# Kernel tuning notes

Hardware: AMD Instinct MI355X
Metric: run time of the kernel (lower is better)

Reference implementation:

```python
import jax, jax.numpy as jnp
import numpy as np

B, L, D = 2, 1024, 512
E = 2
DI = E * D            # d_inner = 1024
N = 16                # d_state
K = 4                 # d_conv
DT_RANK = 32          # ceil(d_model / 16)


def setup_inputs() -> dict:
    key = jax.random.key(0)
    ks = jax.random.split(key, 12)
    s = lambda i, shape, scale=0.02: jax.random.normal(ks[i], shape, jnp.float32) * scale
    return {
        "x": jax.random.normal(ks[0], (B, L, D), jnp.float32),
        # Mamba params (mamba_ssm layout: Linear weights are [out, in])
        "W_in": s(1, (2 * DI, D)),                 # in_proj, bias=False
        "conv_w": s(2, (DI, K), 0.1),              # depthwise conv kernel
        "conv_b": jnp.zeros((DI,), jnp.float32),
        "W_xproj": s(3, (DT_RANK + 2 * N, DI)),    # x_proj, bias=False
        "W_dt": s(4, (DI, DT_RANK), 0.1),
        "b_dt": s(5, (DI,), 0.5),
        "A_log": jnp.log(jnp.broadcast_to(jnp.arange(1, N + 1, dtype=jnp.float32), (DI, N))),
        "D_skip": jnp.ones((DI,), jnp.float32),
        "W_out": s(6, (D, DI)),                    # out_proj, bias=False
        # block params
        "g1": jnp.ones((D,), jnp.float32), "b1": jnp.zeros((D,), jnp.float32),
        "W_ff1": s(7, (2 * D, D)), "b_ff1": jnp.zeros((2 * D,), jnp.float32),
        "W_ff2": s(8, (D, 2 * D)), "b_ff2": jnp.zeros((D,), jnp.float32),
        "g2": jnp.ones((D,), jnp.float32), "b2": jnp.zeros((D,), jnp.float32),
    }


def layernorm(x, g, b, eps=1e-5):
    m = x.mean(-1, keepdims=True)
    v = jnp.mean(jnp.square(x - m), -1, keepdims=True)
    return (x - m) * jax.lax.rsqrt(v + eps) * g + b


def mamba(x, W_in, conv_w, conv_b, W_xproj, W_dt, b_dt, A_log, D_skip, W_out):
    xz = x @ W_in.T                              # [B,L,2*DI]
    u, z = jnp.split(xz, 2, axis=-1)             # each [B,L,DI]
    # causal depthwise conv1d over time
    u_t = u.transpose(0, 2, 1)                   # [B,DI,L]
    conv = jax.lax.conv_general_dilated(
        u_t, conv_w[:, None, :], (1,), [(K - 1, 0)], feature_group_count=DI)
    u = jax.nn.silu(conv.transpose(0, 2, 1) + conv_b)   # [B,L,DI]
    # input-dependent dt, B, C
    x_dbl = u @ W_xproj.T                        # [B,L,DT_RANK+2N]
    dt_r, Bm, Cm = jnp.split(x_dbl, [DT_RANK, DT_RANK + N], axis=-1)
    dt = jax.nn.softplus(dt_r @ W_dt.T + b_dt)   # [B,L,DI]
    A = -jnp.exp(A_log)                          # [DI,N]
    dA = jnp.exp(dt[..., None] * A)                                # [B,L,DI,N]
    dBu = dt[..., None] * Bm[:, :, None, :] * u[..., None]         # [B,L,DI,N]

    def step(h, xs):
        dA_t, dBu_t, C_t = xs
        h = dA_t * h + dBu_t                    # [B,DI,N]
        y = jnp.einsum('bdn,bn->bd', h, C_t)
        return h, y

    h0 = jnp.zeros((B, DI, N), dt.dtype)
    _, ys = jax.lax.scan(step, h0, (dA.transpose(1, 0, 2, 3),
                                    dBu.transpose(1, 0, 2, 3),
                                    Cm.transpose(1, 0, 2)))
    y = ys.transpose(1, 0, 2) + u * D_skip       # [B,L,DI]
    y = y * jax.nn.silu(z)
    return y @ W_out.T                            # [B,L,D]


def reference(x, W_in, conv_w, conv_b, W_xproj, W_dt, b_dt, A_log, D_skip, W_out,
              g1, b1, W_ff1, b_ff1, W_ff2, b_ff2, g2, b2):
    m = mamba(x, W_in, conv_w, conv_b, W_xproj, W_dt, b_dt, A_log, D_skip, W_out)
    res1 = x - m
    r = layernorm(res1, g1, b1)
    ff = jax.nn.gelu(r @ W_ff1.T + b_ff1, approximate=False) @ W_ff2.T + b_ff2
    res2 = r - ff
    out = layernorm(jax.nn.silu(res2), g2, b2)
    return out + x
```

## Files before the change

kernel.cpp:

```cpp
#include <hip/hip_runtime.h>
#include <math.h>

#define BB 2
#define LL 1024
#define DD 512
#define DIN 1024
#define NS 16
#define RNK 32
#define ML (BB*LL)
#define CT 16
#define NC (LL/CT)
#define BDIN (BB*DIN)

typedef unsigned short u16;
typedef unsigned int u32;

__device__ __forceinline__ float sigmoidf_(float v) { return 1.f / (1.f + __expf(-v)); }
__device__ __forceinline__ float siluf_(float v) { return v * sigmoidf_(v); }
__device__ __forceinline__ u16 f2bf(float f) {
  union { float f; u32 u; } c; c.f = f;
  u32 r = c.u + 0x7fffu + ((c.u >> 16) & 1u);
  return (u16)(r >> 16);
}
__device__ __forceinline__ float bf2f(u16 x) {
  union { u32 u; float f; } c; c.u = (u32)x << 16;
  return c.f;
}

__global__ __launch_bounds__(256) void cast_all(const float* __restrict__ x,
                                                const float* __restrict__ Wi,
                                                const float* __restrict__ Wx,
                                                const float* __restrict__ Wd,
                                                const float* __restrict__ Wo,
                                                const float* __restrict__ Wf1,
                                                const float* __restrict__ Wf2,
                                                u16* bx, u16* bWi, u16* bWx, u16* bWd,
                                                u16* bWo, u16* bWf1, u16* bWf2)
{
  int bid = blockIdx.x;
  const float* src; u16* dst; int base;
  if (bid < 512)       { src = x;   dst = bx;   base = 0; }
  else if (bid < 1024) { src = Wi;  dst = bWi;  base = 512; }
  else if (bid < 1056) { src = Wx;  dst = bWx;  base = 1024; }
  else if (bid < 1072) { src = Wd;  dst = bWd;  base = 1056; }
  else if (bid < 1328) { src = Wo;  dst = bWo;  base = 1072; }
  else if (bid < 1584) { src = Wf1; dst = bWf1; base = 1328; }
  else                 { src = Wf2; dst = bWf2; base = 1584; }
  int i = ((bid - base) * 256 + threadIdx.x) * 8;
  float4 v0 = *(const float4*)&src[i];
  float4 v1 = *(const float4*)&src[i + 4];
  union { u16 u[8]; uint4 v; } p;
  p.u[0] = f2bf(v0.x); p.u[1] = f2bf(v0.y); p.u[2] = f2bf(v0.z); p.u[3] = f2bf(v0.w);
  p.u[4] = f2bf(v1.x); p.u[5] = f2bf(v1.y); p.u[6] = f2bf(v1.z); p.u[7] = f2bf(v1.w);
  *(uint4*)&dst[i] = p.v;
}

using bf16x8 = __attribute__((ext_vector_type(8))) short;
using f32x4  = __attribute__((ext_vector_type(4))) float;

template<int BM, int BN, int EPI, typename OT>
__global__ __launch_bounds__(256) void gemm_t(const u16* __restrict__ A,
                                              const u16* __restrict__ W,
                                              const float* __restrict__ bias,
                                              OT* __restrict__ C,
                                              int M, int N, int K)
{
  constexpr int WR = BM / 64;
  constexpr int WC = 4 / WR;
  constexpr int NW = BN / WC;
  constexpr int JJ = NW / 16;
  constexpr int RB = BN / 64;
  __shared__ u16 As[BM][40];
  __shared__ u16 Bs[BN][40];
  const int bm = blockIdx.y * BM, bn = blockIdx.x * BN;
  const int tid = threadIdx.x;
  const int w = tid >> 6, l = tid & 63;
  const int wr = w / WC, wc = w % WC;
  const int lr = l & 15, lh = l >> 4;
  const int sr0 = tid >> 2, sc0 = tid & 3;
  f32x4 acc[4][JJ] = {};
  for (int k0 = 0; k0 < K; k0 += 32) {
    uint4 areg[WR], breg[RB];
#pragma unroll
    for (int i = 0; i < WR; ++i)
      areg[i] = *(const uint4*)&A[(size_t)(bm + sr0 + 64 * i) * K + k0 + sc0 * 8];
#pragma unroll
    for (int i = 0; i < RB; ++i)
      breg[i] = *(const uint4*)&W[(size_t)(bn + sr0 + 64 * i) * K + k0 + sc0 * 8];
    __syncthreads();
#pragma unroll
    for (int i = 0; i < WR; ++i) *(uint4*)&As[sr0 + 64 * i][sc0 * 8] = areg[i];
#pragma unroll
    for (int i = 0; i < RB; ++i) *(uint4*)&Bs[sr0 + 64 * i][sc0 * 8] = breg[i];
    __syncthreads();
    bf16x8 af[4], bfr[JJ];
#pragma unroll
    for (int i = 0; i < 4; ++i) af[i]  = *(bf16x8*)&As[wr * 64 + i * 16 + lr][lh * 8];
#pragma unroll
    for (int j = 0; j < JJ; ++j) bfr[j] = *(bf16x8*)&Bs[wc * NW + j * 16 + lr][lh * 8];
#pragma unroll
    for (int i = 0; i < 4; ++i)
#pragma unroll
      for (int j = 0; j < JJ; ++j)
        acc[i][j] = __builtin_amdgcn_mfma_f32_16x16x32_bf16(af[i], bfr[j], acc[i][j], 0, 0, 0);
  }
#pragma unroll
  for (int i = 0; i < 4; ++i) {
#pragma unroll
    for (int j = 0; j < JJ; ++j) {
      int col = bn + wc * NW + j * 16 + lr;
      float bv = (EPI >= 1) ? bias[col] : 0.f;
#pragma unroll
      for (int r = 0; r < 4; ++r) {
        int row = bm + wr * 64 + i * 16 + lh * 4 + r;
        float t = acc[i][j][r] + bv;
        if (EPI == 2) t = 0.5f * t * (1.f + erff(t * 0.70710678118654752f));
        if (EPI == 3) t = fmaxf(t, 0.f) + log1pf(__expf(-fabsf(t)));
        if constexpr (sizeof(OT) == 2) C[(size_t)row * N + col] = (OT)f2bf(t);
        else                           C[(size_t)row * N + col] = (OT)t;
      }
    }
  }
}

__global__ __launch_bounds__(256) void xproj_mfma(const u16* __restrict__ A,
                                                  const u16* __restrict__ W,
                                                  float* __restrict__ C,
                                                  u16* __restrict__ bdtr)
{
  __shared__ u16 As[128][40];
  __shared__ u16 Bs[64][40];
  const int bm = blockIdx.x * 128;
  const int tid = threadIdx.x;
  const int w = tid >> 6, l = tid & 63;
  const int lr = l & 15, lh = l >> 4;
  const int sr0 = tid >> 2, sc0 = tid & 3;
  f32x4 acc[2][4] = {};
  for (int k0 = 0; k0 < DIN; k0 += 32) {
    uint4 a0 = *(const uint4*)&A[(size_t)(bm + sr0) * DIN + k0 + sc0 * 8];
    uint4 a1 = *(const uint4*)&A[(size_t)(bm + sr0 + 64) * DIN + k0 + sc0 * 8];
    uint4 b0;
    if (sr0 < 64) b0 = *(const uint4*)&W[(size_t)sr0 * DIN + k0 + sc0 * 8];
    __syncthreads();
    *(uint4*)&As[sr0][sc0 * 8] = a0;
    *(uint4*)&As[sr0 + 64][sc0 * 8] = a1;
    if (sr0 < 64) *(uint4*)&Bs[sr0][sc0 * 8] = b0;
    __syncthreads();
    bf16x8 af[2], bfr[4];
#pragma unroll
    for (int i = 0; i < 2; ++i) af[i]  = *(bf16x8*)&As[w * 32 + i * 16 + lr][lh * 8];
#pragma unroll
    for (int j = 0; j < 4; ++j) bfr[j] = *(bf16x8*)&Bs[j * 16 + lr][lh * 8];
#pragma unroll
    for (int i = 0; i < 2; ++i)
#pragma unroll
      for (int j = 0; j < 4; ++j)
        acc[i][j] = __builtin_amdgcn_mfma_f32_16x16x32_bf16(af[i], bfr[j], acc[i][j], 0, 0, 0);
  }
#pragma unroll
  for (int i = 0; i < 2; ++i)
#pragma unroll
    for (int j = 0; j < 4; ++j) {
      int col = j * 16 + lr;
#pragma unroll
      for (int r = 0; r < 4; ++r) {
        int row = bm + w * 32 + i * 16 + lh * 4 + r;
        float v = acc[i][j][r];
        C[(size_t)row * 64 + col] = v;
        if (j < 2) bdtr[(size_t)row * RNK + col] = f2bf(v);
      }
    }
}

__global__ __launch_bounds__(256) void conv_silu(const float* __restrict__ xz,
                                                 const float* __restrict__ conv_w,
                                                 const float* __restrict__ conv_b,
                                                 u16* __restrict__ ucb)
{
  int idx = blockIdx.x * 256 + threadIdx.x;
  int d = idx & (DIN - 1);
  int bl = idx >> 10;
  int l = bl & (LL - 1);
  int b = bl >> 10;
  float acc = conv_b[d];
#pragma unroll
  for (int k = 0; k < 4; ++k) {
    int ls = l - 3 + k;
    float uv = (ls >= 0) ? xz[((size_t)(b * LL + ls)) * (2 * DIN) + d] : 0.f;
    acc = fmaf(uv, conv_w[d * 4 + k], acc);
  }
  ucb[idx] = f2bf(siluf_(acc));
}


__global__ __launch_bounds__(256) void scan_p1(const float* __restrict__ dt,
                                               const u16* __restrict__ ucb,
                                               const float* __restrict__ xdbl,
                                               const float* __restrict__ A_log,
                                               float* __restrict__ apG,
                                               float* __restrict__ hG)
{
  __shared__ float dts[CT][256];
  __shared__ float us[CT][256];
  __shared__ float Bs[CT][NS];
  const int d0 = blockIdx.x * 256, c = blockIdx.y, b = blockIdx.z;
  const int tid = threadIdx.x;
  const int t0 = c * CT;
  for (int i = tid; i < CT * 64; i += 256) {
    int r = i >> 6, col = (i & 63) * 4;
    size_t row = (size_t)(b * LL + t0 + r);
    *(float4*)&dts[r][col] = *(const float4*)&dt[row * DIN + d0 + col];
    ushort4 uv = *(const ushort4*)&ucb[row * DIN + d0 + col];
    float4 uf = { bf2f(uv.x), bf2f(uv.y), bf2f(uv.z), bf2f(uv.w) };
    *(float4*)&us[r][col] = uf;
  }
  { int r = tid >> 4, n = tid & 15;
    Bs[r][n] = xdbl[(size_t)(b * LL + t0 + r) * 64 + 32 + n]; }
  __syncthreads();
  const int d = d0 + tid;
  float Ad[NS];
#pragma unroll
  for (int n = 0; n < NS; ++n) Ad[n] = -__expf(A_log[d * NS + n]);
  float h[NS] = {};
  float sdt = 0.f;
#pragma unroll 4
  for (int t = 0; t < CT; ++t) {
    float dtv = dts[t][tid];
    float dtu = dtv * us[t][tid];
    sdt += dtv;
    float4 B0 = *(float4*)&Bs[t][0],  B1 = *(float4*)&Bs[t][4];
    float4 B2 = *(float4*)&Bs[t][8],  B3 = *(float4*)&Bs[t][12];
    float Bq[NS] = { B0.x, B0.y, B0.z, B0.w, B1.x, B1.y, B1.z, B1.w,
                     B2.x, B2.y, B2.z, B2.w, B3.x, B3.y, B3.z, B3.w };
#pragma unroll
    for (int n = 0; n < NS; ++n) {
      float a = __expf(dtv * Ad[n]);
      h[n] = fmaf(a, h[n], dtu * Bq[n]);
    }
  }
  const int bd = b * DIN + d;
#pragma unroll
  for (int n = 0; n < NS; ++n) {
    apG[((size_t)c * NS + n) * BDIN + bd] = __expf(Ad[n] * sdt);
    hG [((size_t)c * NS + n) * BDIN + bd] = h[n];
  }
}

__global__ __launch_bounds__(128) void scan_p2(const float* __restrict__ apG,
                                               float* __restrict__ hG)
{
  const int idx = blockIdx.x * 128 + threadIdx.x;
  float H = 0.f;
#pragma unroll 16
  for (int c = 0; c < NC; ++c) {
    size_t o = (size_t)c * (NS * BDIN) + idx;
    float ap = apG[o];
    float hl = hG[o];
    hG[o] = H;
    H = fmaf(ap, H, hl);
  }
}

__global__ __launch_bounds__(256) void scan_p3(const float* __restrict__ dt,
                                               const u16* __restrict__ ucb,
                                               const float* __restrict__ xz,
                                               const float* __restrict__ xdbl,
                                               const float* __restrict__ A_log,
                                               const float* __restrict__ D_skip,
                                               const float* __restrict__ hG,
                                               u16* __restrict__ ygb)
{
  __shared__ float dts[CT][256];
  __shared__ float us[CT][256];
  __shared__ float zs[CT][256];
  __shared__ float Bs[CT][NS];
  __shared__ float Cs[CT][NS];
  const int d0 = blockIdx.x * 256, c = blockIdx.y, b = blockIdx.z;
  const int tid = threadIdx.x;
  const int t0 = c * CT;
  for (int i = tid; i < CT * 64; i += 256) {
    int r = i >> 6, col = (i & 63) * 4;
    size_t row = (size_t)(b * LL + t0 + r);
    *(float4*)&dts[r][col] = *(const float4*)&dt[row * DIN + d0 + col];
    ushort4 uv = *(const ushort4*)&ucb[row * DIN + d0 + col];
    float4 uf = { bf2f(uv.x), bf2f(uv.y), bf2f(uv.z), bf2f(uv.w) };
    *(float4*)&us[r][col] = uf;
    *(float4*)&zs[r][col] = *(const float4*)&xz[row * (2 * DIN) + DIN + d0 + col];
  }
  { int r = tid >> 4, n = tid & 15;
    size_t row = (size_t)(b * LL + t0 + r);
    Bs[r][n] = xdbl[row * 64 + 32 + n];
    Cs[r][n] = xdbl[row * 64 + 48 + n]; }
  __syncthreads();
  const int d = d0 + tid;
  const int bd = b * DIN + d;
  float Ad[NS];
#pragma unroll
  for (int n = 0; n < NS; ++n) Ad[n] = -__expf(A_log[d * NS + n]);
  const float Dd = D_skip[d];
  float h[NS];
#pragma unroll
  for (int n = 0; n < NS; ++n) h[n] = hG[((size_t)c * NS + n) * BDIN + bd];
#pragma unroll 2
  for (int t = 0; t < CT; ++t) {
    float dtv = dts[t][tid];
    float ucv = us[t][tid];
    float dtu = dtv * ucv;
    float4 B0 = *(float4*)&Bs[t][0],  B1 = *(float4*)&Bs[t][4];
    float4 B2 = *(float4*)&Bs[t][8],  B3 = *(float4*)&Bs[t][12];
    float4 C0 = *(float4*)&Cs[t][0],  C1 = *(float4*)&Cs[t][4];
    float4 C2 = *(float4*)&Cs[t][8],  C3 = *(float4*)&Cs[t][12];
    float Bq[NS] = { B0.x, B0.y, B0.z, B0.w, B1.x, B1.y, B1.z, B1.w,
                     B2.x, B2.y, B2.z, B2.w, B3.x, B3.y, B3.z, B3.w };
    float Cq[NS] = { C0.x, C0.y, C0.z, C0.w, C1.x, C1.y, C1.z, C1.w,
                     C2.x, C2.y, C2.z, C2.w, C3.x, C3.y, C3.z, C3.w };
    float y = 0.f;
#pragma unroll
    for (int n = 0; n < NS; ++n) {
      float a = __expf(dtv * Ad[n]);
      h[n] = fmaf(a, h[n], dtu * Bq[n]);
      y = fmaf(h[n], Cq[n], y);
    }
    float o = fmaf(ucv, Dd, y) * siluf_(zs[t][tid]);
    ygb[(size_t)(b * LL + t0 + t) * DIN + d0 + tid] = f2bf(o);
  }
}

__global__ __launch_bounds__(256) void ln1_kernel(const float* __restrict__ x,
                                                  const float* __restrict__ m,
                                                  const float* __restrict__ g,
                                                  const float* __restrict__ b,
                                                  float* __restrict__ r,
                                                  u16* __restrict__ rbf)
{
  int row = blockIdx.x;
  int tid = threadIdx.x;
  size_t base = (size_t)row * DD;
  float2 xv = *(const float2*)&x[base + tid * 2];
  float2 mv = *(const float2*)&m[base + tid * 2];
  float v0 = xv.x - mv.x, v1 = xv.y - mv.y;
  float s = v0 + v1, ss = v0 * v0 + v1 * v1;
#pragma unroll
  for (int off = 32; off; off >>= 1) { s += __shfl_down(s, off, 64); ss += __shfl_down(ss, off, 64); }
  __shared__ float sm[8];
  int w = tid >> 6;
  if ((tid & 63) == 0) { sm[w] = s; sm[4 + w] = ss; }
  __syncthreads();
  float S = sm[0] + sm[1] + sm[2] + sm[3];
  float SS = sm[4] + sm[5] + sm[6] + sm[7];
  float mean = S * (1.f / DD);
  float var = SS * (1.f / DD) - mean * mean;
  float rstd = rsqrtf(var + 1e-5f);
  float2 gv = *(const float2*)&g[tid * 2];
  float2 bv = *(const float2*)&b[tid * 2];
  float2 o;
  o.x = (v0 - mean) * rstd * gv.x + bv.x;
  o.y = (v1 - mean) * rstd * gv.y + bv.y;
  *(float2*)&r[base + tid * 2] = o;
  u32 pk = (u32)f2bf(o.x) | ((u32)f2bf(o.y) << 16);
  *(u32*)&rbf[base + tid * 2] = pk;
}

__global__ __launch_bounds__(256) void final_kernel(const float* __restrict__ r,
                                                    const float* __restrict__ ff,
                                                    const float* __restrict__ x,
                                                    const float* __restrict__ g,
                                                    const float* __restrict__ b,
                                                    float* __restrict__ out)
{
  int row = blockIdx.x;
  int tid = threadIdx.x;
  size_t base = (size_t)row * DD;
  float2 rv = *(const float2*)&r[base + tid * 2];
  float2 fv = *(const float2*)&ff[base + tid * 2];
  float v0 = rv.x - fv.x, v1 = rv.y - fv.y;
  v0 = siluf_(v0); v1 = siluf_(v1);
  float s = v0 + v1, ss = v0 * v0 + v1 * v1;
#pragma unroll
  for (int off = 32; off; off >>= 1) { s += __shfl_down(s, off, 64); ss += __shfl_down(ss, off, 64); }
  __shared__ float sm[8];
  int w = tid >> 6;
  if ((tid & 63) == 0) { sm[w] = s; sm[4 + w] = ss; }
  __syncthreads();
  float S = sm[0] + sm[1] + sm[2] + sm[3];
  float SS = sm[4] + sm[5] + sm[6] + sm[7];
  float mean = S * (1.f / DD);
  float var = SS * (1.f / DD) - mean * mean;
  float rstd = rsqrtf(var + 1e-5f);
  float2 gv = *(const float2*)&g[tid * 2];
  float2 bv = *(const float2*)&b[tid * 2];
  float2 xv = *(const float2*)&x[base + tid * 2];
  float2 o;
  o.x = (v0 - mean) * rstd * gv.x + bv.x + xv.x;
  o.y = (v1 - mean) * rstd * gv.y + bv.y + xv.y;
  *(float2*)&out[base + tid * 2] = o;
}

extern "C" void kernel_launch(void* const* d_in, const int* in_sizes, int n_in,
                              void* d_out, int out_size, void* d_ws, size_t ws_size,
                              hipStream_t stream)
{
  const float* x      = (const float*)d_in[0];
  const float* W_in   = (const float*)d_in[1];
  const float* conv_w = (const float*)d_in[2];
  const float* conv_b = (const float*)d_in[3];
  const float* W_xp   = (const float*)d_in[4];
  const float* W_dt   = (const float*)d_in[5];
  const float* b_dt   = (const float*)d_in[6];
  const float* A_log  = (const float*)d_in[7];
  const float* D_skip = (const float*)d_in[8];
  const float* W_out  = (const float*)d_in[9];
  const float* g1     = (const float*)d_in[10];
  const float* b1     = (const float*)d_in[11];
  const float* W_ff1  = (const float*)d_in[12];
  const float* b_ff1  = (const float*)d_in[13];
  const float* W_ff2  = (const float*)d_in[14];
  const float* b_ff2  = (const float*)d_in[15];
  const float* g2     = (const float*)d_in[16];
  const float* b2     = (const float*)d_in[17];
  float* out = (float*)d_out;

  float* ws = (float*)d_ws;
  float* xz     = ws;
  float* xdbl   = ws + 4194304;
  float* dtb    = ws + 4325376;
  float* apG    = ws + 6422528;
  float* hG     = ws + 8519680;
  float* mb     = ws + 10616832;
  float* rb     = ws + 11665408;
  u16*   bffh   = (u16*)(ws + 12713984);
  u16*   ygb    = (u16*)(ws + 13762560);
  u16*   ucb    = (u16*)(ws + 14811136);
  u16*   brb    = (u16*)(ws + 15859712);
  u16*   bdtr   = (u16*)(ws + 16384000);
  u16*   bx     = (u16*)(ws + 16416768);
  u16*   bW_in  = (u16*)(ws + 16941056);
  u16*   bWxp   = (u16*)(ws + 17989632);
  u16*   bW_dt  = (u16*)(ws + 18022400);
  u16*   bW_out = (u16*)(ws + 18038784);
  u16*   bW_ff1 = (u16*)(ws + 18300928);
  u16*   bW_ff2 = (u16*)(ws + 18563072);

  cast_all<<<1840, 256, 0, stream>>>(x, W_in, W_xp, W_dt, W_out, W_ff1, W_ff2,
                                     bx, bW_in, bWxp, bW_dt, bW_out, bW_ff1, bW_ff2);
  gemm_t<128, 64, 0, float><<<dim3(2 * DIN / 64, ML / 128), 256, 0, stream>>>(
      bx, bW_in, nullptr, xz, ML, 2 * DIN, DD);
  conv_silu<<<(ML * DIN) / 256, 256, 0, stream>>>(xz, conv_w, conv_b, ucb);
  xproj_mfma<<<ML / 128, 256, 0, stream>>>(ucb, bWxp, xdbl, bdtr);
  gemm_t<128, 64, 3, float><<<dim3(DIN / 64, ML / 128), 256, 0, stream>>>(
      bdtr, bW_dt, b_dt, dtb, ML, DIN, RNK);
  scan_p1<<<dim3(DIN / 256, NC, BB), 256, 0, stream>>>(dtb, ucb, xdbl, A_log, apG, hG);
  scan_p2<<<(NS * BDIN) / 128, 128, 0, stream>>>(apG, hG);
  scan_p3<<<dim3(DIN / 256, NC, BB), 256, 0, stream>>>(dtb, ucb, xz, xdbl, A_log, D_skip,
                                                       hG, ygb);
  gemm_t<64, 64, 0, float><<<dim3(DD / 64, ML / 64), 256, 0, stream>>>(
      ygb, bW_out, nullptr, mb, ML, DD, DIN);
  ln1_kernel<<<ML, 256, 0, stream>>>(x, mb, g1, b1, rb, brb);
  gemm_t<128, 64, 2, u16><<<dim3(DIN / 64, ML / 128), 256, 0, stream>>>(
      brb, bW_ff1, b_ff1, bffh, ML, DIN, DD);
  gemm_t<64, 64, 1, float><<<dim3(DD / 64, ML / 64), 256, 0, stream>>>(
      bffh, bW_ff2, b_ff2, mb, ML, DD, DIN);
  final_kernel<<<ML, 256, 0, stream>>>(rb, mb, x, g2, b2, out);
}
```

Measured before the change: 172.9 us.

## Fuse three scan phases into one cooperative kernel and store xz in bf16

Replaces the three-kernel chunked selective scan with a single cooperative kernel that uses grid-wide syncs between the local chunk pass, the cross-chunk carry propagation and the output pass. The dt, u, z, B and C tiles are loaded into shared memory once and reused across all phases. This removes two launches and the reloads done by the third phase. Separately, the in_proj GEMM now writes xz as bf16, halving traffic for conv_silu and the z reads. The cooperative launch needs all 512 blocks resident at once, grid syncs add latency, and bf16 z/u lowers precision.

```diff
diff --git a/kernel.cpp b/kernel.cpp
--- a/kernel.cpp
+++ b/kernel.cpp
@@ -1,5 +1,8 @@
 #include <hip/hip_runtime.h>
+#include <hip/hip_cooperative_groups.h>
 #include <math.h>
+
+namespace cg = cooperative_groups;
 
 #define BB 2
 #define LL 1024
@@ -172,7 +175,7 @@
     }
 }
 
-__global__ __launch_bounds__(256) void conv_silu(const float* __restrict__ xz,
+__global__ __launch_bounds__(256) void conv_silu(const u16* __restrict__ xzb,
                                                  const float* __restrict__ conv_w,
                                                  const float* __restrict__ conv_b,
                                                  u16* __restrict__ ucb)
@@ -186,89 +189,21 @@
 #pragma unroll
   for (int k = 0; k < 4; ++k) {
     int ls = l - 3 + k;
-    float uv = (ls >= 0) ? xz[((size_t)(b * LL + ls)) * (2 * DIN) + d] : 0.f;
+    float uv = (ls >= 0) ? bf2f(xzb[((size_t)(b * LL + ls)) * (2 * DIN) + d]) : 0.f;
     acc = fmaf(uv, conv_w[d * 4 + k], acc);
   }
   ucb[idx] = f2bf(siluf_(acc));
 }
 
-
-__global__ __launch_bounds__(256) void scan_p1(const float* __restrict__ dt,
-                                               const u16* __restrict__ ucb,
-                                               const float* __restrict__ xdbl,
-                                               const float* __restrict__ A_log,
-                                               float* __restrict__ apG,
-                                               float* __restrict__ hG)
-{
-  __shared__ float dts[CT][256];
-  __shared__ float us[CT][256];
-  __shared__ float Bs[CT][NS];
-  const int d0 = blockIdx.x * 256, c = blockIdx.y, b = blockIdx.z;
-  const int tid = threadIdx.x;
-  const int t0 = c * CT;
-  for (int i = tid; i < CT * 64; i += 256) {
-    int r = i >> 6, col = (i & 63) * 4;
-    size_t row = (size_t)(b * LL + t0 + r);
-    *(float4*)&dts[r][col] = *(const float4*)&dt[row * DIN + d0 + col];
-    ushort4 uv = *(const ushort4*)&ucb[row * DIN + d0 + col];
-    float4 uf = { bf2f(uv.x), bf2f(uv.y), bf2f(uv.z), bf2f(uv.w) };
-    *(float4*)&us[r][col] = uf;
-  }
-  { int r = tid >> 4, n = tid & 15;
-    Bs[r][n] = xdbl[(size_t)(b * LL + t0 + r) * 64 + 32 + n]; }
-  __syncthreads();
-  const int d = d0 + tid;
-  float Ad[NS];
-#pragma unroll
-  for (int n = 0; n < NS; ++n) Ad[n] = -__expf(A_log[d * NS + n]);
-  float h[NS] = {};
-  float sdt = 0.f;
-#pragma unroll 4
-  for (int t = 0; t < CT; ++t) {
-    float dtv = dts[t][tid];
-    float dtu = dtv * us[t][tid];
-    sdt += dtv;
-    float4 B0 = *(float4*)&Bs[t][0],  B1 = *(float4*)&Bs[t][4];
-    float4 B2 = *(float4*)&Bs[t][8],  B3 = *(float4*)&Bs[t][12];
-    float Bq[NS] = { B0.x, B0.y, B0.z, B0.w, B1.x, B1.y, B1.z, B1.w,
-                     B2.x, B2.y, B2.z, B2.w, B3.x, B3.y, B3.z, B3.w };
-#pragma unroll
-    for (int n = 0; n < NS; ++n) {
-      float a = __expf(dtv * Ad[n]);
-      h[n] = fmaf(a, h[n], dtu * Bq[n]);
-    }
-  }
-  const int bd = b * DIN + d;
-#pragma unroll
-  for (int n = 0; n < NS; ++n) {
-    apG[((size_t)c * NS + n) * BDIN + bd] = __expf(Ad[n] * sdt);
-    hG [((size_t)c * NS + n) * BDIN + bd] = h[n];
-  }
-}
-
-__global__ __launch_bounds__(128) void scan_p2(const float* __restrict__ apG,
-                                               float* __restrict__ hG)
-{
-  const int idx = blockIdx.x * 128 + threadIdx.x;
-  float H = 0.f;
-#pragma unroll 16
-  for (int c = 0; c < NC; ++c) {
-    size_t o = (size_t)c * (NS * BDIN) + idx;
-    float ap = apG[o];
-    float hl = hG[o];
-    hG[o] = H;
-    H = fmaf(ap, H, hl);
-  }
-}
-
-__global__ __launch_bounds__(256) void scan_p3(const float* __restrict__ dt,
-                                               const u16* __restrict__ ucb,
-                                               const float* __restrict__ xz,
-                                               const float* __restrict__ xdbl,
-                                               const float* __restrict__ A_log,
-                                               const float* __restrict__ D_skip,
-                                               const float* __restrict__ hG,
-                                               u16* __restrict__ ygb)
+__global__ __launch_bounds__(256) void scan_fused(const float* __restrict__ dt,
+                                                  const u16* __restrict__ ucb,
+                                                  const u16* __restrict__ xzb,
+                                                  const float* __restrict__ xdbl,
+                                                  const float* __restrict__ A_log,
+                                                  const float* __restrict__ D_skip,
+                                                  float* __restrict__ apG,
+                                                  float* __restrict__ hG,
+                                                  u16* __restrict__ ygb)
 {
   __shared__ float dts[CT][256];
   __shared__ float us[CT][256];
@@ -285,7 +220,9 @@
     ushort4 uv = *(const ushort4*)&ucb[row * DIN + d0 + col];
     float4 uf = { bf2f(uv.x), bf2f(uv.y), bf2f(uv.z), bf2f(uv.w) };
     *(float4*)&us[r][col] = uf;
-    *(float4*)&zs[r][col] = *(const float4*)&xz[row * (2 * DIN) + DIN + d0 + col];
+    ushort4 zv = *(const ushort4*)&xzb[row * (2 * DIN) + DIN + d0 + col];
+    float4 zf = { bf2f(zv.x), bf2f(zv.y), bf2f(zv.z), bf2f(zv.w) };
+    *(float4*)&zs[r][col] = zf;
   }
   { int r = tid >> 4, n = tid & 15;
     size_t row = (size_t)(b * LL + t0 + r);
@@ -297,32 +234,74 @@
   float Ad[NS];
 #pragma unroll
   for (int n = 0; n < NS; ++n) Ad[n] = -__expf(A_log[d * NS + n]);
-  const float Dd = D_skip[d];
-  float h[NS];
-#pragma unroll
-  for (int n = 0; n < NS; ++n) h[n] = hG[((size_t)c * NS + n) * BDIN + bd];
+  {
+    float h[NS] = {};
+    float sdt = 0.f;
+#pragma unroll 4
+    for (int t = 0; t < CT; ++t) {
+      float dtv = dts[t][tid];
+      float dtu = dtv * us[t][tid];
+      sdt += dtv;
+      float4 B0 = *(float4*)&Bs[t][0],  B1 = *(float4*)&Bs[t][4];
+      float4 B2 = *(float4*)&Bs[t][8],  B3 = *(float4*)&Bs[t][12];
+      float Bq[NS] = { B0.x, B0.y, B0.z, B0.w, B1.x, B1.y, B1.z, B1.w,
+                       B2.x, B2.y, B2.z, B2.w, B3.x, B3.y, B3.z, B3.w };
+#pragma unroll
+      for (int n = 0; n < NS; ++n) {
+        float a = __expf(dtv * Ad[n]);
+        h[n] = fmaf(a, h[n], dtu * Bq[n]);
+      }
+    }
+#pragma unroll
+    for (int n = 0; n < NS; ++n) {
+      apG[((size_t)c * NS + n) * BDIN + bd] = __expf(Ad[n] * sdt);
+      hG [((size_t)c * NS + n) * BDIN + bd] = h[n];
+    }
+  }
+  cg::this_grid().sync();
+  {
+    const int gl = ((blockIdx.z * gridDim.y + blockIdx.y) * gridDim.x + blockIdx.x) * 256 + tid;
+    if (gl < NS * BDIN) {
+      float H = 0.f;
+#pragma unroll 16
+      for (int c2 = 0; c2 < NC; ++c2) {
+        size_t o = (size_t)c2 * (NS * BDIN) + gl;
+        float ap = apG[o];
+        float hl = hG[o];
+        hG[o] = H;
+        H = fmaf(ap, H, hl);
+      }
+    }
+  }
+  cg::this_grid().sync();
+  {
+    const float Dd = D_skip[d];
+    float h[NS];
+#pragma unroll
+    for (int n = 0; n < NS; ++n) h[n] = hG[((size_t)c * NS + n) * BDIN + bd];
 #pragma unroll 2
-  for (int t = 0; t < CT; ++t) {
-    float dtv = dts[t][tid];
-    float ucv = us[t][tid];
-    float dtu = dtv * ucv;
-    float4 B0 = *(float4*)&Bs[t][0],  B1 = *(float4*)&Bs[t][4];
-    float4 B2 = *(float4*)&Bs[t][8],  B3 = *(float4*)&Bs[t][12];
-    float4 C0 = *(float4*)&Cs[t][0],  C1 = *(float4*)&Cs[t][4];
-    float4 C2 = *(float4*)&Cs[t][8],  C3 = *(float4*)&Cs[t][12];
-    float Bq[NS] = { B0.x, B0.y, B0.z, B0.w, B1.x, B1.y, B1.z, B1.w,
-                     B2.x, B2.y, B2.z, B2.w, B3.x, B3.y, B3.z, B3.w };
-    float Cq[NS] = { C0.x, C0.y, C0.z, C0.w, C1.x, C1.y, C1.z, C1.w,
-                     C2.x, C2.y, C2.z, C2.w, C3.x, C3.y, C3.z, C3.w };
-    float y = 0.f;
-#pragma unroll
-    for (int n = 0; n < NS; ++n) {
-      float a = __expf(dtv * Ad[n]);
-      h[n] = fmaf(a, h[n], dtu * Bq[n]);
-      y = fmaf(h[n], Cq[n], y);
-    }
-    float o = fmaf(ucv, Dd, y) * siluf_(zs[t][tid]);
-    ygb[(size_t)(b * LL + t0 + t) * DIN + d0 + tid] = f2bf(o);
+    for (int t = 0; t < CT; ++t) {
+      float dtv = dts[t][tid];
+      float ucv = us[t][tid];
+      float dtu = dtv * ucv;
+      float4 B0 = *(float4*)&Bs[t][0],  B1 = *(float4*)&Bs[t][4];
+      float4 B2 = *(float4*)&Bs[t][8],  B3 = *(float4*)&Bs[t][12];
+      float4 C0 = *(float4*)&Cs[t][0],  C1 = *(float4*)&Cs[t][4];
+      float4 C2 = *(float4*)&Cs[t][8],  C3 = *(float4*)&Cs[t][12];
+      float Bq[NS] = { B0.x, B0.y, B0.z, B0.w, B1.x, B1.y, B1.z, B1.w,
+                       B2.x, B2.y, B2.z, B2.w, B3.x, B3.y, B3.z, B3.w };
+      float Cq[NS] = { C0.x, C0.y, C0.z, C0.w, C1.x, C1.y, C1.z, C1.w,
+                       C2.x, C2.y, C2.z, C2.w, C3.x, C3.y, C3.z, C3.w };
+      float y = 0.f;
+#pragma unroll
+      for (int n = 0; n < NS; ++n) {
+        float a = __expf(dtv * Ad[n]);
+        h[n] = fmaf(a, h[n], dtu * Bq[n]);
+        y = fmaf(h[n], Cq[n], y);
+      }
+      float o = fmaf(ucv, Dd, y) * siluf_(zs[t][tid]);
+      ygb[(size_t)(b * LL + t0 + t) * DIN + d0 + tid] = f2bf(o);
+    }
   }
 }
 
@@ -421,7 +400,7 @@
   float* out = (float*)d_out;
 
   float* ws = (float*)d_ws;
-  float* xz     = ws;
+  u16*   xzb    = (u16*)ws;
   float* xdbl   = ws + 4194304;
   float* dtb    = ws + 4325376;
   float* apG    = ws + 6422528;
@@ -443,16 +422,18 @@
 
   cast_all<<<1840, 256, 0, stream>>>(x, W_in, W_xp, W_dt, W_out, W_ff1, W_ff2,
                                      bx, bW_in, bWxp, bW_dt, bW_out, bW_ff1, bW_ff2);
-  gemm_t<128, 64, 0, float><<<dim3(2 * DIN / 64, ML / 128), 256, 0, stream>>>(
-      bx, bW_in, nullptr, xz, ML, 2 * DIN, DD);
-  conv_silu<<<(ML * DIN) / 256, 256, 0, stream>>>(xz, conv_w, conv_b, ucb);
+  gemm_t<128, 64, 0, u16><<<dim3(2 * DIN / 64, ML / 128), 256, 0, stream>>>(
+      bx, bW_in, nullptr, xzb, ML, 2 * DIN, DD);
+  conv_silu<<<(ML * DIN) / 256, 256, 0, stream>>>(xzb, conv_w, conv_b, ucb);
   xproj_mfma<<<ML / 128, 256, 0, stream>>>(ucb, bWxp, xdbl, bdtr);
   gemm_t<128, 64, 3, float><<<dim3(DIN / 64, ML / 128), 256, 0, stream>>>(
       bdtr, bW_dt, b_dt, dtb, ML, DIN, RNK);
-  scan_p1<<<dim3(DIN / 256, NC, BB), 256, 0, stream>>>(dtb, ucb, xdbl, A_log, apG, hG);
-  scan_p2<<<(NS * BDIN) / 128, 128, 0, stream>>>(apG, hG);
-  scan_p3<<<dim3(DIN / 256, NC, BB), 256, 0, stream>>>(dtb, ucb, xz, xdbl, A_log, D_skip,
-                                                       hG, ygb);
+  {
+    void* args[] = { (void*)&dtb, (void*)&ucb, (void*)&xzb, (void*)&xdbl, (void*)&A_log,
+                     (void*)&D_skip, (void*)&apG, (void*)&hG, (void*)&ygb };
+    hipLaunchCooperativeKernel((const void*)scan_fused, dim3(DIN / 256, NC, BB),
+                               dim3(256), args, 0, stream);
+  }
   gemm_t<64, 64, 0, float><<<dim3(DD / 64, ML / 64), 256, 0, stream>>>(
       ygb, bW_out, nullptr, mb, ML, DD, DIN);
   ln1_kernel<<<ML, 256, 0, stream>>>(x, mb, g1, b1, rb, brb);
```

Measured after the change: 286.0 us. 65.4% more time.
